# Kernel optimization log

Hardware: AMD Instinct MI355X
Metric: run time of the kernel (lower is better)

The kernel has to match this reference:

```python
import jax, jax.numpy as jnp
import numpy as np

D = 256
NHEAD = 4
T = 8
TOTAL_STEPS = 64
EPS = 1e-5


def _ln(x, g, b):
    m = jnp.mean(x, -1, keepdims=True)
    v = jnp.mean((x - m) ** 2, -1, keepdims=True)
    return (x - m) / jnp.sqrt(v + EPS) * g + b


def setup_inputs() -> dict:
    key = jax.random.key(0)
    ks = iter(jax.random.split(key, 64))

    def W(shape):
        return jax.random.normal(next(ks), shape, jnp.float32) * 0.02

    B = 1024
    inp = {
        "fen_tokens": jax.random.randint(next(ks), (B, 77), 0, 128, jnp.int32),
        "uci_token": jax.random.randint(next(ks), (B, 1), 0, 1968, jnp.int32),
        "fen_emb_w": W((128, D)),
        "uci_emb_w": W((1968, D)),
        "pos_emb_w": W((78, D)),
        "tl_wqkv": W((4, D, 3 * D)), "tl_bqkv": jnp.zeros((4, 3 * D)),
        "tl_wo": W((4, D, D)), "tl_bo": jnp.zeros((4, D)),
        "tl_ln1_g": jnp.ones((4, D)), "tl_ln1_b": jnp.zeros((4, D)),
        "tl_w1": W((4, D, 2048)), "tl_b1": jnp.zeros((4, 2048)),
        "tl_w2": W((4, 2048, D)), "tl_b2": jnp.zeros((4, D)),
        "tl_ln2_g": jnp.ones((4, D)), "tl_ln2_b": jnp.zeros((4, D)),
        "post_ln_g": jnp.ones(D), "post_ln_b": jnp.zeros(D),
        "pool_w1": W((D, D)), "pool_b1": jnp.zeros(D),
        "pool_w2": W((D, D)), "pool_b2": jnp.zeros(D),
        "L_w1": W((3 * D, D)), "L_b1": jnp.zeros(D),
        "L_w2": W((D, D)), "L_b2": jnp.zeros(D),
        "L_ln_g": jnp.ones(D), "L_ln_b": jnp.zeros(D),
        "H_w1": W((2 * D, D)), "H_b1": jnp.zeros(D),
        "H_w2": W((D, D)), "H_b2": jnp.zeros(D),
        "H_ln_g": jnp.ones(D), "H_ln_b": jnp.zeros(D),
        "vh_ln_g": jnp.ones(D), "vh_ln_b": jnp.zeros(D),
        "vh_w1": W((D, D)), "vh_b1": jnp.zeros(D),
        "vh_w2": W((D, 128)), "vh_b2": jnp.zeros(128),
    }
    return inp


def _forward(fen_tokens, uci_token, fen_emb_w, uci_emb_w, pos_emb_w,
             tl_wqkv, tl_bqkv, tl_wo, tl_bo, tl_ln1_g, tl_ln1_b,
             tl_w1, tl_b1, tl_w2, tl_b2, tl_ln2_g, tl_ln2_b,
             post_ln_g, post_ln_b, pool_w1, pool_b1, pool_w2, pool_b2,
             L_w1, L_b1, L_w2, L_b2, L_ln_g, L_ln_b,
             H_w1, H_b1, H_w2, H_b2, H_ln_g, H_ln_b,
             vh_ln_g, vh_ln_b, vh_w1, vh_b1, vh_w2, vh_b2):
    B = fen_tokens.shape[0]
    hd = D // NHEAD
    # embed: [B,77,D] cat [B,1,D] -> [B,78,D], plus positional embedding
    x = jnp.concatenate([fen_emb_w[fen_tokens], uci_emb_w[uci_token[:, 0]][:, None, :]], axis=1)
    x = x + pos_emb_w[None]
    # 4-layer post-norm transformer encoder (relu FFN, d_ff=2048)
    for l in range(4):
        qkv = x @ tl_wqkv[l] + tl_bqkv[l]
        q, k, v = jnp.split(qkv, 3, axis=-1)
        q = q.reshape(B, -1, NHEAD, hd).transpose(0, 2, 1, 3)
        k = k.reshape(B, -1, NHEAD, hd).transpose(0, 2, 1, 3)
        v = v.reshape(B, -1, NHEAD, hd).transpose(0, 2, 1, 3)
        att = jax.nn.softmax(jnp.einsum('bhqd,bhkd->bhqk', q, k) / jnp.sqrt(jnp.float32(hd)), axis=-1)
        o = jnp.einsum('bhqk,bhkd->bhqd', att, v).transpose(0, 2, 1, 3).reshape(B, -1, D)
        x = _ln(x + o @ tl_wo[l] + tl_bo[l], tl_ln1_g[l], tl_ln1_b[l])
        ff = jax.nn.relu(x @ tl_w1[l] + tl_b1[l]) @ tl_w2[l] + tl_b2[l]
        x = _ln(x + ff, tl_ln2_g[l], tl_ln2_b[l])
    x = _ln(x, post_ln_g, post_ln_b)
    pooled = jax.nn.relu(jax.nn.relu(x @ pool_w1 + pool_b1) @ pool_w2 + pool_b2)
    out = pooled.mean(axis=1)  # [B,D]

    def l_net(t):
        return _ln(jax.nn.relu(jax.nn.relu(t @ L_w1 + L_b1) @ L_w2 + L_b2), L_ln_g, L_ln_b)

    def h_net(t):
        return _ln(jax.nn.relu(jax.nn.relu(t @ H_w1 + H_b1) @ H_w2 + H_b2), H_ln_g, H_ln_b)

    z0 = jnp.zeros((B, D), x.dtype)

    def step(carry, i):
        zL, zH = carry
        zL = l_net(jnp.concatenate([zL, zH, out], axis=-1))
        zH_new = h_net(jnp.concatenate([zH, zL], axis=-1))
        zH = jnp.where(((i + 1) % T) == 0, zH_new, zH)
        return (zL, zH), None

    # first 63 steps run under torch.no_grad -> stop_gradient on the scan result
    (zL, zH), _ = jax.lax.scan(step, (z0, z0), jnp.arange(TOTAL_STEPS - 1))
    zL = jax.lax.stop_gradient(zL)
    zH = jax.lax.stop_gradient(zH)
    zL = l_net(jnp.concatenate([zL, zH, out], axis=-1))
    zH = h_net(jnp.concatenate([zH, zL], axis=-1))
    vh = _ln(zH, vh_ln_g, vh_ln_b)
    return jax.nn.relu(vh @ vh_w1 + vh_b1) @ vh_w2 + vh_b2  # [B, num_bins]


def reference(fen_tokens, uci_token, fen_emb_w, uci_emb_w, pos_emb_w,
              tl_wqkv, tl_bqkv, tl_wo, tl_bo, tl_ln1_g, tl_ln1_b,
              tl_w1, tl_b1, tl_w2, tl_b2, tl_ln2_g, tl_ln2_b,
              post_ln_g, post_ln_b, pool_w1, pool_b1, pool_w2, pool_b2,
              L_w1, L_b1, L_w2, L_b2, L_ln_g, L_ln_b,
              H_w1, H_b1, H_w2, H_b2, H_ln_g, H_ln_b,
              vh_ln_g, vh_ln_b, vh_w1, vh_b1, vh_w2, vh_b2):
    return _forward(fen_tokens, uci_token, fen_emb_w, uci_emb_w, pos_emb_w,
                    tl_wqkv, tl_bqkv, tl_wo, tl_bo, tl_ln1_g, tl_ln1_b,
                    tl_w1, tl_b1, tl_w2, tl_b2, tl_ln2_g, tl_ln2_b,
                    post_ln_g, post_ln_b, pool_w1, pool_b1, pool_w2, pool_b2,
                    L_w1, L_b1, L_w2, L_b2, L_ln_g, L_ln_b,
                    H_w1, H_b1, H_w2, H_b2, H_ln_g, H_ln_b,
                    vh_ln_g, vh_ln_b, vh_w1, vh_b1, vh_w2, vh_b2)
```

## Files before the change

### kernel.cpp

```cpp
#include <hip/hip_runtime.h>
#include <cstdint>
#include <cstddef>

typedef unsigned short u16;
typedef short s8v __attribute__((ext_vector_type(8)));
typedef float f32x4 __attribute__((ext_vector_type(4)));
typedef u16 u16x4 __attribute__((ext_vector_type(4)));

#define DEV __device__ __forceinline__

DEV u16 f2bf(float f) {
  union { float f; uint32_t u; } a; a.f = f;
  uint32_t u = a.u;
  return (u16)((u + 0x7fffu + ((u >> 16) & 1u)) >> 16);
}
DEV float bf2f(u16 h) {
  union { uint32_t u; float f; } a; a.u = ((uint32_t)h) << 16;
  return a.f;
}
DEV void f2bf_split(float v, u16& hi, u16& lo) {
  hi = f2bf(v);
  lo = f2bf(v - bf2f(hi));
}

__global__ __launch_bounds__(256) void k_transpose(const float* __restrict__ W,
                                                   u16* __restrict__ WThi,
                                                   u16* __restrict__ WTlo, int K, int N) {
  __shared__ float tile[32][33];
  int k0 = blockIdx.x * 32, n0 = blockIdx.y * 32;
  int tx = threadIdx.x & 31, ty = threadIdx.x >> 5;
#pragma unroll
  for (int i = 0; i < 32; i += 8)
    tile[ty + i][tx] = W[(size_t)(k0 + ty + i) * N + n0 + tx];
  __syncthreads();
#pragma unroll
  for (int i = 0; i < 32; i += 8) {
    float w = tile[tx][ty + i];
    u16 hi, lo; f2bf_split(w, hi, lo);
    size_t idx = (size_t)(n0 + ty + i) * K + k0 + tx;
    WThi[idx] = hi;
    WTlo[idx] = lo;
  }
}

__global__ __launch_bounds__(256) void k_embed(const int* __restrict__ fen,
                                               const int* __restrict__ uci,
                                               const float* __restrict__ femb,
                                               const float* __restrict__ uemb,
                                               const float* __restrict__ pemb,
                                               float* __restrict__ xf,
                                               u16* __restrict__ xhi, u16* __restrict__ xlo,
                                               int b0) {
  int row = blockIdx.x;
  int c = threadIdx.x;
  int bl = row / 78, p = row % 78;
  int b = b0 + bl;
  int tok;
  const float* e;
  if (p < 77) { tok = fen[b * 77 + p]; e = femb; }
  else        { tok = uci[b];          e = uemb; }
  float v = e[(size_t)tok * 256 + c] + pemb[p * 256 + c];
  size_t idx = (size_t)row * 256 + c;
  xf[idx] = v;
  u16 hi, lo; f2bf_split(v, hi, lo);
  xhi[idx] = hi;
  xlo[idx] = lo;
}

template <bool RELU, bool OUT_F32, bool OUT_SPLIT>
__global__ __launch_bounds__(256) void k_gemm(const u16* __restrict__ Ahi,
                                              const u16* __restrict__ Alo,
                                              const u16* __restrict__ Bhi,
                                              const u16* __restrict__ Blo,
                                              const float* __restrict__ bias,
                                              float* __restrict__ Cf,
                                              u16* __restrict__ Chi, u16* __restrict__ Clo,
                                              int M, int N, int K) {
  __shared__ __align__(16) u16 As[128][72];
  __shared__ __align__(16) u16 Bs[128][72];
  const int tid = threadIdx.x;
  const int wid = tid >> 6, lane = tid & 63;
  const int wr = wid >> 1, wc = wid & 1;
  const int m0 = blockIdx.x * 128, n0 = blockIdx.y * 128;
  f32x4 acc[4][4] = {};
  const int sr = tid >> 3;
  const int sc = (tid & 7) * 8;

  for (int p = 0; p < 3; p++) {
    const u16* __restrict__ A = (p == 2) ? Alo : Ahi;
    const u16* __restrict__ B = (p == 1) ? Blo : Bhi;
    for (int kt = 0; kt < K; kt += 64) {
#pragma unroll
      for (int i = 0; i < 4; i++) {
        int row = sr + i * 32;
        *(s8v*)&As[row][sc] = *(const s8v*)&A[(size_t)(m0 + row) * K + kt + sc];
        *(s8v*)&Bs[row][sc] = *(const s8v*)&B[(size_t)(n0 + row) * K + kt + sc];
      }
      __syncthreads();
#pragma unroll
      for (int kk = 0; kk < 2; kk++) {
        s8v af[4], bf[4];
#pragma unroll
        for (int i = 0; i < 4; i++) {
          af[i] = *(const s8v*)&As[wr * 64 + i * 16 + (lane & 15)][kk * 32 + (lane >> 4) * 8];
          bf[i] = *(const s8v*)&Bs[wc * 64 + i * 16 + (lane & 15)][kk * 32 + (lane >> 4) * 8];
        }
#pragma unroll
        for (int i = 0; i < 4; i++)
#pragma unroll
          for (int j = 0; j < 4; j++)
            acc[i][j] = __builtin_amdgcn_mfma_f32_16x16x32_bf16(af[i], bf[j], acc[i][j], 0, 0, 0);
      }
      __syncthreads();
    }
  }
#pragma unroll
  for (int j = 0; j < 4; j++) {
    int col = n0 + wc * 64 + j * 16 + (lane & 15);
    float bv = bias[col];
#pragma unroll
    for (int i = 0; i < 4; i++) {
#pragma unroll
      for (int r = 0; r < 4; r++) {
        int row = m0 + wr * 64 + i * 16 + (lane >> 4) * 4 + r;
        float v = acc[i][j][r] + bv;
        if (RELU) v = fmaxf(v, 0.f);
        size_t idx = (size_t)row * N + col;
        if (OUT_F32) Cf[idx] = v;
        if (OUT_SPLIT) {
          u16 hi, lo; f2bf_split(v, hi, lo);
          Chi[idx] = hi;
          Clo[idx] = lo;
        }
      }
    }
  }
}

__global__ __launch_bounds__(128) void k_attn(const float* __restrict__ qkvf,
                                              u16* __restrict__ ohi, u16* __restrict__ olo) {
  __shared__ float Ks[78][68];
  __shared__ float Vs[78][68];
  __shared__ float Ss[78][79];
  const int bl = blockIdx.x >> 2, h = blockIdx.x & 3;
  const int tid = threadIdx.x;
  const size_t rowbase = (size_t)bl * 78;
  for (int ci = tid; ci < 1248; ci += 128) {
    int row = ci >> 4, c4 = (ci & 15) * 4;
    const float* kp = &qkvf[(rowbase + row) * 768 + 256 + h * 64 + c4];
    *(float4*)&Ks[row][c4] = *(const float4*)kp;
    *(float4*)&Vs[row][c4] = *(const float4*)(kp + 256);
  }
  __syncthreads();
  const int q = tid;
  if (q < 78) {
    float qv[64];
    const float* qp = &qkvf[(rowbase + q) * 768 + h * 64];
#pragma unroll
    for (int d4 = 0; d4 < 64; d4 += 4) {
      float4 t = *(const float4*)&qp[d4];
      qv[d4] = t.x; qv[d4 + 1] = t.y; qv[d4 + 2] = t.z; qv[d4 + 3] = t.w;
    }
    float mx = -1e30f;
    for (int k = 0; k < 78; k++) {
      float s = 0.f;
#pragma unroll
      for (int d = 0; d < 64; d++) s += qv[d] * Ks[k][d];
      s *= 0.125f;
      Ss[q][k] = s;
      mx = fmaxf(mx, s);
    }
    float sum = 0.f;
    for (int k = 0; k < 78; k++) { float e = __expf(Ss[q][k] - mx); Ss[q][k] = e; sum += e; }
    float inv = 1.f / sum;
    float ov[64];
#pragma unroll
    for (int d = 0; d < 64; d++) ov[d] = 0.f;
    for (int k = 0; k < 78; k++) {
      float p = Ss[q][k];
#pragma unroll
      for (int d = 0; d < 64; d++) ov[d] += p * Vs[k][d];
    }
    size_t obase = (rowbase + q) * 256 + h * 64;
#pragma unroll
    for (int d8 = 0; d8 < 64; d8 += 8) {
      s8v whi, wlo;
#pragma unroll
      for (int j = 0; j < 8; j++) {
        u16 hi, lo; f2bf_split(ov[d8 + j] * inv, hi, lo);
        whi[j] = (short)hi; wlo[j] = (short)lo;
      }
      *(s8v*)&ohi[obase + d8] = whi;
      *(s8v*)&olo[obase + d8] = wlo;
    }
  }
}

template <bool ADD>
__global__ __launch_bounds__(256) void k_addln(const float* __restrict__ x,
                                               const float* __restrict__ t,
                                               const float* __restrict__ g,
                                               const float* __restrict__ b,
                                               float* __restrict__ xo,
                                               u16* __restrict__ xhi, u16* __restrict__ xlo) {
  int row = blockIdx.x * 4 + (threadIdx.x >> 6);
  int lane = threadIdx.x & 63;
  const float* xr = x + (size_t)row * 256;
  float4 v = *(const float4*)&xr[lane * 4];
  if (ADD) {
    float4 tv = *(const float4*)&t[(size_t)row * 256 + lane * 4];
    v.x += tv.x; v.y += tv.y; v.z += tv.z; v.w += tv.w;
  }
  float s = v.x + v.y + v.z + v.w;
  float q = v.x * v.x + v.y * v.y + v.z * v.z + v.w * v.w;
#pragma unroll
  for (int off = 32; off; off >>= 1) { s += __shfl_down(s, off); q += __shfl_down(q, off); }
  s = __shfl(s, 0); q = __shfl(q, 0);
  float mean = s * (1.f / 256.f);
  float var = q * (1.f / 256.f) - mean * mean;
  float rstd = rsqrtf(var + 1e-5f);
  float4 gg = *(const float4*)&g[lane * 4];
  float4 bb = *(const float4*)&b[lane * 4];
  float o0 = (v.x - mean) * rstd * gg.x + bb.x;
  float o1 = (v.y - mean) * rstd * gg.y + bb.y;
  float o2 = (v.z - mean) * rstd * gg.z + bb.z;
  float o3 = (v.w - mean) * rstd * gg.w + bb.w;
  size_t base = (size_t)row * 256 + lane * 4;
  *(float4*)&xo[base] = make_float4(o0, o1, o2, o3);
  u16 h0, l0, h1, l1, h2, l2, h3, l3;
  f2bf_split(o0, h0, l0); f2bf_split(o1, h1, l1);
  f2bf_split(o2, h2, l2); f2bf_split(o3, h3, l3);
  u16x4 vh = { h0, h1, h2, h3 };
  u16x4 vl = { l0, l1, l2, l3 };
  *(u16x4*)&xhi[base] = vh;
  *(u16x4*)&xlo[base] = vl;
}

__global__ __launch_bounds__(256) void k_mean(const float* __restrict__ p2,
                                              float* __restrict__ out, int b0) {
  int bl = blockIdx.x, d = threadIdx.x;
  const float* base = p2 + (size_t)bl * 78 * 256 + d;
  float s = 0.f;
#pragma unroll 13
  for (int p = 0; p < 78; p++) s += base[(size_t)p * 256];
  out[(size_t)(b0 + bl) * 256 + d] = s * (1.f / 78.f);
}

__global__ __launch_bounds__(256) void k_zero(float* p, int n) {
  int i = blockIdx.x * 256 + threadIdx.x;
  if (i < n) p[i] = 0.f;
}

__global__ __launch_bounds__(256) void k_lbase(const float* __restrict__ zH,
                                               const float* __restrict__ out,
                                               const float* __restrict__ W1,
                                               const float* __restrict__ b1,
                                               float* __restrict__ baseL) {
  int r0 = blockIdx.x * 4, col = threadIdx.x;
  __shared__ float t[4][512];
#pragma unroll
  for (int i = 0; i < 4; i++) {
    t[i][col] = zH[(size_t)(r0 + i) * 256 + col];
    t[i][256 + col] = out[(size_t)(r0 + i) * 256 + col];
  }
  __syncthreads();
  float acc[4];
#pragma unroll
  for (int i = 0; i < 4; i++) acc[i] = b1[col];
  for (int k = 0; k < 512; k++) {
    float w = W1[(size_t)(256 + k) * 256 + col];
#pragma unroll
    for (int i = 0; i < 4; i++) acc[i] += t[i][k] * w;
  }
#pragma unroll
  for (int i = 0; i < 4; i++) baseL[(size_t)(r0 + i) * 256 + col] = acc[i];
}

DEV void row_ln_stats(float a2[4], int col, float (*redS)[4], float (*redQ)[4],
                      float mean[4], float rstd[4]) {
  int wid = col >> 6, lane = col & 63;
#pragma unroll
  for (int i = 0; i < 4; i++) {
    float s = a2[i], q = a2[i] * a2[i];
#pragma unroll
    for (int off = 32; off; off >>= 1) { s += __shfl_down(s, off); q += __shfl_down(q, off); }
    if (lane == 0) { redS[i][wid] = s; redQ[i][wid] = q; }
  }
  __syncthreads();
#pragma unroll
  for (int i = 0; i < 4; i++) {
    float s = redS[i][0] + redS[i][1] + redS[i][2] + redS[i][3];
    float q = redQ[i][0] + redQ[i][1] + redQ[i][2] + redQ[i][3];
    mean[i] = s * (1.f / 256.f);
    float var = q * (1.f / 256.f) - mean[i] * mean[i];
    rstd[i] = rsqrtf(var + 1e-5f);
  }
}

__global__ __launch_bounds__(256) void k_lstep(float* __restrict__ zL,
                                               const float* __restrict__ baseL,
                                               const float* __restrict__ W1,
                                               const float* __restrict__ W2,
                                               const float* __restrict__ b2,
                                               const float* __restrict__ g,
                                               const float* __restrict__ bb) {
  int r0 = blockIdx.x * 4, col = threadIdx.x;
  __shared__ float t[4][256];
  __shared__ float h1[4][256];
  __shared__ float redS[4][4], redQ[4][4];
#pragma unroll
  for (int i = 0; i < 4; i++) t[i][col] = zL[(size_t)(r0 + i) * 256 + col];
  __syncthreads();
  float acc[4];
#pragma unroll
  for (int i = 0; i < 4; i++) acc[i] = baseL[(size_t)(r0 + i) * 256 + col];
  for (int k = 0; k < 256; k++) {
    float w = W1[(size_t)k * 256 + col];
#pragma unroll
    for (int i = 0; i < 4; i++) acc[i] += t[i][k] * w;
  }
#pragma unroll
  for (int i = 0; i < 4; i++) h1[i][col] = fmaxf(acc[i], 0.f);
  __syncthreads();
  float a2[4];
#pragma unroll
  for (int i = 0; i < 4; i++) a2[i] = b2[col];
  for (int k = 0; k < 256; k++) {
    float w = W2[(size_t)k * 256 + col];
#pragma unroll
    for (int i = 0; i < 4; i++) a2[i] += h1[i][k] * w;
  }
#pragma unroll
  for (int i = 0; i < 4; i++) a2[i] = fmaxf(a2[i], 0.f);
  float mean[4], rstd[4];
  row_ln_stats(a2, col, redS, redQ, mean, rstd);
#pragma unroll
  for (int i = 0; i < 4; i++)
    zL[(size_t)(r0 + i) * 256 + col] = (a2[i] - mean[i]) * rstd[i] * g[col] + bb[col];
}

__global__ __launch_bounds__(256) void k_hstep(float* __restrict__ zH,
                                               const float* __restrict__ zL,
                                               const float* __restrict__ W1,
                                               const float* __restrict__ b1,
                                               const float* __restrict__ W2,
                                               const float* __restrict__ b2,
                                               const float* __restrict__ g,
                                               const float* __restrict__ bb) {
  int r0 = blockIdx.x * 4, col = threadIdx.x;
  __shared__ float t[4][512];
  __shared__ float h1[4][256];
  __shared__ float redS[4][4], redQ[4][4];
#pragma unroll
  for (int i = 0; i < 4; i++) {
    t[i][col] = zH[(size_t)(r0 + i) * 256 + col];
    t[i][256 + col] = zL[(size_t)(r0 + i) * 256 + col];
  }
  __syncthreads();
  float acc[4];
#pragma unroll
  for (int i = 0; i < 4; i++) acc[i] = b1[col];
  for (int k = 0; k < 512; k++) {
    float w = W1[(size_t)k * 256 + col];
#pragma unroll
    for (int i = 0; i < 4; i++) acc[i] += t[i][k] * w;
  }
#pragma unroll
  for (int i = 0; i < 4; i++) h1[i][col] = fmaxf(acc[i], 0.f);
  __syncthreads();
  float a2[4];
#pragma unroll
  for (int i = 0; i < 4; i++) a2[i] = b2[col];
  for (int k = 0; k < 256; k++) {
    float w = W2[(size_t)k * 256 + col];
#pragma unroll
    for (int i = 0; i < 4; i++) a2[i] += h1[i][k] * w;
  }
#pragma unroll
  for (int i = 0; i < 4; i++) a2[i] = fmaxf(a2[i], 0.f);
  float mean[4], rstd[4];
  row_ln_stats(a2, col, redS, redQ, mean, rstd);
#pragma unroll
  for (int i = 0; i < 4; i++)
    zH[(size_t)(r0 + i) * 256 + col] = (a2[i] - mean[i]) * rstd[i] * g[col] + bb[col];
}

__global__ __launch_bounds__(256) void k_vh(const float* __restrict__ zH,
                                            const float* __restrict__ g,
                                            const float* __restrict__ bb,
                                            const float* __restrict__ W1,
                                            const float* __restrict__ b1,
                                            const float* __restrict__ W2,
                                            const float* __restrict__ b2,
                                            float* __restrict__ out) {
  int r0 = blockIdx.x * 4, col = threadIdx.x;
  __shared__ float t[4][256];
  __shared__ float h1[4][256];
  __shared__ float redS[4][4], redQ[4][4];
  float v[4];
#pragma unroll
  for (int i = 0; i < 4; i++) v[i] = zH[(size_t)(r0 + i) * 256 + col];
  float mean[4], rstd[4];
  row_ln_stats(v, col, redS, redQ, mean, rstd);
#pragma unroll
  for (int i = 0; i < 4; i++) t[i][col] = (v[i] - mean[i]) * rstd[i] * g[col] + bb[col];
  __syncthreads();
  float acc[4];
#pragma unroll
  for (int i = 0; i < 4; i++) acc[i] = b1[col];
  for (int k = 0; k < 256; k++) {
    float w = W1[(size_t)k * 256 + col];
#pragma unroll
    for (int i = 0; i < 4; i++) acc[i] += t[i][k] * w;
  }
#pragma unroll
  for (int i = 0; i < 4; i++) h1[i][col] = fmaxf(acc[i], 0.f);
  __syncthreads();
  if (col < 128) {
    float a2[4];
#pragma unroll
    for (int i = 0; i < 4; i++) a2[i] = b2[col];
    for (int k = 0; k < 256; k++) {
      float w = W2[(size_t)k * 128 + col];
#pragma unroll
      for (int i = 0; i < 4; i++) a2[i] += h1[i][k] * w;
    }
#pragma unroll
    for (int i = 0; i < 4; i++) out[(size_t)(r0 + i) * 128 + col] = a2[i];
  }
}

extern "C" void kernel_launch(void* const* d_in, const int* in_sizes, int n_in,
                              void* d_out, int out_size, void* d_ws, size_t ws_size,
                              hipStream_t stream) {
  (void)in_sizes; (void)n_in; (void)out_size;
  const int* fen = (const int*)d_in[0];
  const int* uci = (const int*)d_in[1];
  const float* femb = (const float*)d_in[2];
  const float* uemb = (const float*)d_in[3];
  const float* pemb = (const float*)d_in[4];
  const float* wqkv = (const float*)d_in[5];
  const float* bqkv = (const float*)d_in[6];
  const float* wo_ = (const float*)d_in[7];
  const float* bo_ = (const float*)d_in[8];
  const float* ln1g = (const float*)d_in[9];
  const float* ln1b = (const float*)d_in[10];
  const float* w1_ = (const float*)d_in[11];
  const float* b1_ = (const float*)d_in[12];
  const float* w2_ = (const float*)d_in[13];
  const float* b2_ = (const float*)d_in[14];
  const float* ln2g = (const float*)d_in[15];
  const float* ln2b = (const float*)d_in[16];
  const float* postg = (const float*)d_in[17];
  const float* postb = (const float*)d_in[18];
  const float* pw1 = (const float*)d_in[19];
  const float* pb1 = (const float*)d_in[20];
  const float* pw2 = (const float*)d_in[21];
  const float* pb2 = (const float*)d_in[22];
  const float* Lw1 = (const float*)d_in[23];
  const float* Lb1 = (const float*)d_in[24];
  const float* Lw2 = (const float*)d_in[25];
  const float* Lb2 = (const float*)d_in[26];
  const float* Llng = (const float*)d_in[27];
  const float* Llnb = (const float*)d_in[28];
  const float* Hw1 = (const float*)d_in[29];
  const float* Hb1 = (const float*)d_in[30];
  const float* Hw2 = (const float*)d_in[31];
  const float* Hb2 = (const float*)d_in[32];
  const float* Hlng = (const float*)d_in[33];
  const float* Hlnb = (const float*)d_in[34];
  const float* vhg = (const float*)d_in[35];
  const float* vhb = (const float*)d_in[36];
  const float* vw1 = (const float*)d_in[37];
  const float* vb1 = (const float*)d_in[38];
  const float* vw2 = (const float*)d_in[39];
  const float* vb2 = (const float*)d_in[40];

  char* p = (char*)d_ws;
  auto alloc = [&](size_t bytes) -> void* {
    void* r = (void*)p;
    p += (bytes + 255) & ~(size_t)255;
    return r;
  };
  float* outf = (float*)alloc(1024 * 256 * 4);
  float* baseL = (float*)alloc(1024 * 256 * 4);
  float* zLH = (float*)alloc(2 * 1024 * 256 * 4);
  float* zL = zLH;
  float* zH = zLH + 1024 * 256;
  u16* wqThi = (u16*)alloc((size_t)4 * 768 * 256 * 2);
  u16* wqTlo = (u16*)alloc((size_t)4 * 768 * 256 * 2);
  u16* woThi = (u16*)alloc((size_t)4 * 256 * 256 * 2);
  u16* woTlo = (u16*)alloc((size_t)4 * 256 * 256 * 2);
  u16* w1Thi = (u16*)alloc((size_t)4 * 2048 * 256 * 2);
  u16* w1Tlo = (u16*)alloc((size_t)4 * 2048 * 256 * 2);
  u16* w2Thi = (u16*)alloc((size_t)4 * 256 * 2048 * 2);
  u16* w2Tlo = (u16*)alloc((size_t)4 * 256 * 2048 * 2);
  u16* pw1Thi = (u16*)alloc((size_t)256 * 256 * 2);
  u16* pw1Tlo = (u16*)alloc((size_t)256 * 256 * 2);
  u16* pw2Thi = (u16*)alloc((size_t)256 * 256 * 2);
  u16* pw2Tlo = (u16*)alloc((size_t)256 * 256 * 2);

  size_t fixed = (size_t)(p - (char*)d_ws);
  int NC = 0;
  for (int c : {8, 16, 4, 2, 1}) {
    size_t Mc_ = (size_t)(1024 / c) * 78;
    if (fixed + Mc_ * 15360 + (size_t)(1 << 20) <= ws_size) { NC = c; break; }
  }
  if (!NC) NC = 16;
  const int Bc = 1024 / NC;
  const size_t Mc = (size_t)Bc * 78;

  float* xf = (float*)alloc(Mc * 256 * 4);
  float* tmp = (float*)alloc(Mc * 256 * 4);
  u16* xhi = (u16*)alloc(Mc * 256 * 2);
  u16* xlo = (u16*)alloc(Mc * 256 * 2);
  float* qkvf = (float*)alloc(Mc * 768 * 4);
  u16* ohi = (u16*)alloc(Mc * 256 * 2);
  u16* olo = (u16*)alloc(Mc * 256 * 2);
  u16* hhi = (u16*)alloc(Mc * 2048 * 2);
  u16* hlo = (u16*)alloc(Mc * 2048 * 2);

  auto tr = [&](const float* W, u16* WThi, u16* WTlo, int K, int N) {
    k_transpose<<<dim3(K / 32, N / 32), 256, 0, stream>>>(W, WThi, WTlo, K, N);
  };
  for (int l = 0; l < 4; l++) {
    tr(wqkv + (size_t)l * 256 * 768, wqThi + (size_t)l * 768 * 256,
       wqTlo + (size_t)l * 768 * 256, 256, 768);
    tr(wo_ + (size_t)l * 256 * 256, woThi + (size_t)l * 256 * 256,
       woTlo + (size_t)l * 256 * 256, 256, 256);
    tr(w1_ + (size_t)l * 256 * 2048, w1Thi + (size_t)l * 2048 * 256,
       w1Tlo + (size_t)l * 2048 * 256, 256, 2048);
    tr(w2_ + (size_t)l * 2048 * 256, w2Thi + (size_t)l * 256 * 2048,
       w2Tlo + (size_t)l * 256 * 2048, 2048, 256);
  }
  tr(pw1, pw1Thi, pw1Tlo, 256, 256);
  tr(pw2, pw2Thi, pw2Tlo, 256, 256);

  const int MT = (int)(Mc / 128);
  for (int ch = 0; ch < NC; ch++) {
    int b0 = ch * Bc;
    k_embed<<<(int)Mc, 256, 0, stream>>>(fen, uci, femb, uemb, pemb, xf, xhi, xlo, b0);
    for (int l = 0; l < 4; l++) {
      k_gemm<false, true, false><<<dim3(MT, 6), 256, 0, stream>>>(
          xhi, xlo, wqThi + (size_t)l * 768 * 256, wqTlo + (size_t)l * 768 * 256,
          bqkv + l * 768, qkvf, nullptr, nullptr, (int)Mc, 768, 256);
      k_attn<<<Bc * 4, 128, 0, stream>>>(qkvf, ohi, olo);
      k_gemm<false, true, false><<<dim3(MT, 2), 256, 0, stream>>>(
          ohi, olo, woThi + (size_t)l * 256 * 256, woTlo + (size_t)l * 256 * 256,
          bo_ + l * 256, tmp, nullptr, nullptr, (int)Mc, 256, 256);
      k_addln<true><<<(int)(Mc / 4), 256, 0, stream>>>(
          xf, tmp, ln1g + l * 256, ln1b + l * 256, xf, xhi, xlo);
      k_gemm<true, false, true><<<dim3(MT, 16), 256, 0, stream>>>(
          xhi, xlo, w1Thi + (size_t)l * 2048 * 256, w1Tlo + (size_t)l * 2048 * 256,
          b1_ + l * 2048, nullptr, hhi, hlo, (int)Mc, 2048, 256);
      k_gemm<false, true, false><<<dim3(MT, 2), 256, 0, stream>>>(
          hhi, hlo, w2Thi + (size_t)l * 256 * 2048, w2Tlo + (size_t)l * 256 * 2048,
          b2_ + l * 256, tmp, nullptr, nullptr, (int)Mc, 256, 2048);
      k_addln<true><<<(int)(Mc / 4), 256, 0, stream>>>(
          xf, tmp, ln2g + l * 256, ln2b + l * 256, xf, xhi, xlo);
    }
    k_addln<false><<<(int)(Mc / 4), 256, 0, stream>>>(xf, nullptr, postg, postb, xf, xhi, xlo);
    k_gemm<true, false, true><<<dim3(MT, 2), 256, 0, stream>>>(
        xhi, xlo, pw1Thi, pw1Tlo, pb1, nullptr, ohi, olo, (int)Mc, 256, 256);
    k_gemm<true, true, false><<<dim3(MT, 2), 256, 0, stream>>>(
        ohi, olo, pw2Thi, pw2Tlo, pb2, tmp, nullptr, nullptr, (int)Mc, 256, 256);
    k_mean<<<Bc, 256, 0, stream>>>(tmp, outf, b0);
  }

  k_zero<<<(2 * 1024 * 256) / 256, 256, 0, stream>>>(zLH, 2 * 1024 * 256);
  for (int st = 0; st < 64; st++) {
    if ((st & 7) == 0)
      k_lbase<<<256, 256, 0, stream>>>(zH, outf, Lw1, Lb1, baseL);
    k_lstep<<<256, 256, 0, stream>>>(zL, baseL, Lw1, Lw2, Lb2, Llng, Llnb);
    if ((st & 7) == 7)
      k_hstep<<<256, 256, 0, stream>>>(zH, zL, Hw1, Hb1, Hw2, Hb2, Hlng, Hlnb);
  }
  k_vh<<<256, 256, 0, stream>>>(zH, vhg, vhb, vw1, vb1, vw2, vb2, (float*)d_out);
}
```

Baseline: 10.99 ms.

## Fuse three split-bf16 GEMM passes into one K loop and prefer fewer batch chunks

The GEMM no longer makes three separate passes over K (hi*hi, hi*lo, lo*hi). It now loads the hi and lo tiles of A and B together into shared memory and issues all three MFMAs per fragment in a single K loop. This cuts global loads and syncs, and lets each tile feed three MFMAs, at the cost of twice the LDS per block (which may lower occupancy) and more fragment registers. The chunk selection now prefers the largest chunk that fits the workspace (fewest chunks) instead of starting at 8, which means fewer, larger launches but more workspace.

Result: slower. 15.19 ms (+38.2%).

```diff
diff --git a/kernel.cpp b/kernel.cpp
--- a/kernel.cpp
+++ b/kernel.cpp
@@ -76,8 +76,10 @@
                                               float* __restrict__ Cf,
                                               u16* __restrict__ Chi, u16* __restrict__ Clo,
                                               int M, int N, int K) {
-  __shared__ __align__(16) u16 As[128][72];
-  __shared__ __align__(16) u16 Bs[128][72];
+  __shared__ __align__(16) u16 Ah[128][72];
+  __shared__ __align__(16) u16 Al[128][72];
+  __shared__ __align__(16) u16 Bh[128][72];
+  __shared__ __align__(16) u16 Bl[128][72];
   const int tid = threadIdx.x;
   const int wid = tid >> 6, lane = tid & 63;
   const int wr = wid >> 1, wc = wid & 1;
@@ -86,33 +88,39 @@
   const int sr = tid >> 3;
   const int sc = (tid & 7) * 8;
 
-  for (int p = 0; p < 3; p++) {
-    const u16* __restrict__ A = (p == 2) ? Alo : Ahi;
-    const u16* __restrict__ B = (p == 1) ? Blo : Bhi;
-    for (int kt = 0; kt < K; kt += 64) {
+  for (int kt = 0; kt < K; kt += 64) {
+#pragma unroll
+    for (int i = 0; i < 4; i++) {
+      int row = sr + i * 32;
+      size_t ga = (size_t)(m0 + row) * K + kt + sc;
+      size_t gb = (size_t)(n0 + row) * K + kt + sc;
+      *(s8v*)&Ah[row][sc] = *(const s8v*)&Ahi[ga];
+      *(s8v*)&Al[row][sc] = *(const s8v*)&Alo[ga];
+      *(s8v*)&Bh[row][sc] = *(const s8v*)&Bhi[gb];
+      *(s8v*)&Bl[row][sc] = *(const s8v*)&Blo[gb];
+    }
+    __syncthreads();
+#pragma unroll
+    for (int kk = 0; kk < 2; kk++) {
+      s8v ah[4], al[4], bh[4], bl[4];
+      const int fr = lane & 15, fc = kk * 32 + (lane >> 4) * 8;
 #pragma unroll
       for (int i = 0; i < 4; i++) {
-        int row = sr + i * 32;
-        *(s8v*)&As[row][sc] = *(const s8v*)&A[(size_t)(m0 + row) * K + kt + sc];
-        *(s8v*)&Bs[row][sc] = *(const s8v*)&B[(size_t)(n0 + row) * K + kt + sc];
+        ah[i] = *(const s8v*)&Ah[wr * 64 + i * 16 + fr][fc];
+        al[i] = *(const s8v*)&Al[wr * 64 + i * 16 + fr][fc];
+        bh[i] = *(const s8v*)&Bh[wc * 64 + i * 16 + fr][fc];
+        bl[i] = *(const s8v*)&Bl[wc * 64 + i * 16 + fr][fc];
       }
-      __syncthreads();
-#pragma unroll
-      for (int kk = 0; kk < 2; kk++) {
-        s8v af[4], bf[4];
-#pragma unroll
-        for (int i = 0; i < 4; i++) {
-          af[i] = *(const s8v*)&As[wr * 64 + i * 16 + (lane & 15)][kk * 32 + (lane >> 4) * 8];
-          bf[i] = *(const s8v*)&Bs[wc * 64 + i * 16 + (lane & 15)][kk * 32 + (lane >> 4) * 8];
+#pragma unroll
+      for (int i = 0; i < 4; i++)
+#pragma unroll
+        for (int j = 0; j < 4; j++) {
+          acc[i][j] = __builtin_amdgcn_mfma_f32_16x16x32_bf16(ah[i], bh[j], acc[i][j], 0, 0, 0);
+          acc[i][j] = __builtin_amdgcn_mfma_f32_16x16x32_bf16(ah[i], bl[j], acc[i][j], 0, 0, 0);
+          acc[i][j] = __builtin_amdgcn_mfma_f32_16x16x32_bf16(al[i], bh[j], acc[i][j], 0, 0, 0);
         }
-#pragma unroll
-        for (int i = 0; i < 4; i++)
-#pragma unroll
-          for (int j = 0; j < 4; j++)
-            acc[i][j] = __builtin_amdgcn_mfma_f32_16x16x32_bf16(af[i], bf[j], acc[i][j], 0, 0, 0);
-      }
-      __syncthreads();
-    }
+    }
+    __syncthreads();
   }
 #pragma unroll
   for (int j = 0; j < 4; j++) {
@@ -501,12 +509,11 @@
   u16* pw2Tlo = (u16*)alloc((size_t)256 * 256 * 2);
 
   size_t fixed = (size_t)(p - (char*)d_ws);
-  int NC = 0;
-  for (int c : {8, 16, 4, 2, 1}) {
+  int NC = 16;
+  for (int c : {1, 2, 4, 8, 16}) {
     size_t Mc_ = (size_t)(1024 / c) * 78;
     if (fixed + Mc_ * 15360 + (size_t)(1 << 20) <= ws_size) { NC = c; break; }
   }
-  if (!NC) NC = 16;
   const int Bc = 1024 / NC;
   const size_t Mc = (size_t)Bc * 78;
 
```
